# Kernel tuning notes

Hardware: AMD Instinct MI355X
Metric: run time of the kernel (lower is better)

## Reference

```python
import jax, jax.numpy as jnp
import numpy as np

EMBED_DIM = 1024
NUM_HEADS = 16
HEAD_DIM = EMBED_DIM // NUM_HEADS
SCALING = (1.0 / HEAD_DIM) ** 0.5


def setup_inputs() -> dict:
    key = jax.random.key(0)
    ks = jax.random.split(key, 9)
    d = EMBED_DIM
    return {
        "hidden_states": jax.random.normal(ks[0], (4, 2048, d), dtype=jnp.float32),
        "q_w": jax.random.normal(ks[1], (d, d), dtype=jnp.float32) * 0.02,
        "q_b": jax.random.normal(ks[2], (d,), dtype=jnp.float32) * 0.02,
        "k_w": jax.random.normal(ks[3], (d, d), dtype=jnp.float32) * 0.02,
        "k_b": jax.random.normal(ks[4], (d,), dtype=jnp.float32) * 0.02,
        "v_w": jax.random.normal(ks[5], (d, d), dtype=jnp.float32) * 0.02,
        "v_b": jax.random.normal(ks[6], (d,), dtype=jnp.float32) * 0.02,
        "out_w": jax.random.normal(ks[7], (d, d), dtype=jnp.float32) * 0.02,
        "out_b": jax.random.normal(ks[8], (d,), dtype=jnp.float32) * 0.02,
    }


def _shape(x, bsz, seq, nh, hd):
    # [B, T, E] -> [B, H, T, Hd]
    return x.reshape(bsz, seq, nh, hd).transpose(0, 2, 1, 3)


def reference(hidden_states, q_w, q_b, k_w, k_b, v_w, v_b, out_w, out_b):
    bsz, tgt_len, _ = hidden_states.shape
    # torch Linear: y = x @ W.T + b; query scaled by sqrt(1/head_dim)
    q = (hidden_states @ q_w.T + q_b) * SCALING
    k = hidden_states @ k_w.T + k_b
    v = hidden_states @ v_w.T + v_b
    q = _shape(q, bsz, tgt_len, NUM_HEADS, HEAD_DIM)
    k = _shape(k, bsz, tgt_len, NUM_HEADS, HEAD_DIM)
    v = _shape(v, bsz, tgt_len, NUM_HEADS, HEAD_DIM)
    # [B, H, T, S]
    attn_weights = jnp.einsum("bhtd,bhsd->bhts", q, k)
    attn_weights = jax.nn.softmax(attn_weights, axis=-1)
    # [B, H, T, Hd] -> [B, T, E]
    attn_output = jnp.einsum("bhts,bhsd->bhtd", attn_weights, v)
    attn_output = attn_output.transpose(0, 2, 1, 3).reshape(bsz, tgt_len, EMBED_DIM)
    return attn_output @ out_w.T + out_b
```

## Files before the change

kernel.cpp:

```cpp
#include <hip/hip_runtime.h>
#include <hip/hip_bf16.h>
#include <cstdint>
#include <math.h>

typedef uint16_t u16;
typedef __attribute__((ext_vector_type(8))) short short8;
typedef __attribute__((ext_vector_type(4))) float floatx4;
typedef __attribute__((ext_vector_type(16))) float floatx16;

__device__ __forceinline__ float bf2f(u16 u) {
  return __uint_as_float(((uint32_t)u) << 16);
}
__device__ __forceinline__ u16 f2bf(float f) {
  uint32_t u = __float_as_uint(f);
  u += 0x7FFF + ((u >> 16) & 1);
  return (u16)(u >> 16);
}

__device__ __forceinline__ void glds16(const void* g, void* l) {
  __builtin_amdgcn_global_load_lds(
      (const __attribute__((address_space(1))) void*)g,
      (__attribute__((address_space(3))) void*)l, 16, 0, 0);
}

__device__ __forceinline__ bool detect_fp32(const u16* __restrict__ hs) {
  int big = 0;
#pragma unroll
  for (int i = 0; i < 128; ++i) {
    const int e = (hs[i] >> 7) & 0xFF;
    big += (e >= 140);
  }
  return big > 0;
}

__device__ __forceinline__ void conv_blk(
    const void* __restrict__ src, u16* __restrict__ dst, int i, bool f32)
{
  if (f32) {
    const float4 v = ((const float4*)src)[i];
    ushort4 d;
    d.x = f2bf(v.x); d.y = f2bf(v.y); d.z = f2bf(v.z); d.w = f2bf(v.w);
    ((ushort4*)dst)[i] = d;
  } else {
    ((ushort4*)dst)[i] = ((const ushort4*)src)[i];
  }
}

__global__ __launch_bounds__(256) void convert_all(
    const void* __restrict__ hs, const void* __restrict__ qw,
    const void* __restrict__ kw, const void* __restrict__ vw,
    const void* __restrict__ ow, const void* __restrict__ qb,
    const void* __restrict__ kb, const void* __restrict__ vb,
    const void* __restrict__ ob,
    u16* __restrict__ d_hs, u16* __restrict__ d_qw, u16* __restrict__ d_kw,
    u16* __restrict__ d_vw, u16* __restrict__ d_ow, u16* __restrict__ d_qb,
    u16* __restrict__ d_kb, u16* __restrict__ d_vb, u16* __restrict__ d_ob)
{
  const bool f32 = detect_fp32((const u16*)hs);
  const int bid = blockIdx.x;
  const int tid = threadIdx.x;
  if (bid < 8192) {
    conv_blk(hs, d_hs, bid * 256 + tid, f32);
  } else if (bid < 8192 + 4096) {
    const int w = (bid - 8192) >> 10;
    const int i = ((bid - 8192) & 1023) * 256 + tid;
    const void* s = (w == 0) ? qw : (w == 1) ? kw : (w == 2) ? vw : ow;
    u16* d        = (w == 0) ? d_qw : (w == 1) ? d_kw : (w == 2) ? d_vw : d_ow;
    conv_blk(s, d, i, f32);
  } else {
    const int w = bid - 12288;
    const void* s = (w == 0) ? qb : (w == 1) ? kb : (w == 2) ? vb : ob;
    u16* d        = (w == 0) ? d_qb : (w == 1) ? d_kb : (w == 2) ? d_vb : d_ob;
    conv_blk(s, d, tid, f32);
  }
}

template <int MODE>
__device__ __forceinline__ void gemm_body(
    const u16* __restrict__ A, const u16* __restrict__ W,
    const u16* __restrict__ bias, void* __restrict__ vout,
    float scale, u16* As, u16* Bs, int bx, int by, bool f32out)
{
  constexpr int KD = 1024;
  const int tid  = threadIdx.x;
  const int lane = tid & 63;
  const int l15  = lane & 15;
  const int quad = lane >> 4;
  const int wid  = tid >> 6;
  const int bm = by * 128, bn = bx * 128;
  const int wm = (wid >> 1) * 64, wn = (wid & 1) * 64;

  floatx4 acc[4][4];
#pragma unroll
  for (int i = 0; i < 4; ++i)
#pragma unroll
    for (int j = 0; j < 4; ++j)
#pragma unroll
      for (int r = 0; r < 4; ++r) acc[i][j][r] = 0.0f;

  const int c0 = tid, c1 = tid + 256;
  const u16* Ag0 = A + (size_t)(bm + (c0 >> 2)) * KD + (c0 & 3) * 8;
  const u16* Ag1 = A + (size_t)(bm + (c1 >> 2)) * KD + (c1 & 3) * 8;
  const u16* Wg0 = W + (size_t)(bn + (c0 >> 2)) * KD + (c0 & 3) * 8;
  const u16* Wg1 = W + (size_t)(bn + (c1 >> 2)) * KD + (c1 & 3) * 8;
  u16* As0 = As + c0 * 8;  u16* As1 = As + c1 * 8;
  u16* Bs0 = Bs + c0 * 8;  u16* Bs1 = Bs + c1 * 8;

  for (int kt = 0; kt < KD / 32; ++kt) {
    const int ko = kt * 32;
    glds16(Ag0 + ko, As0);
    glds16(Ag1 + ko, As1);
    glds16(Wg0 + ko, Bs0);
    glds16(Wg1 + ko, Bs1);
    __syncthreads();
    short8 af[4], bf[4];
#pragma unroll
    for (int mb = 0; mb < 4; ++mb)
      af[mb] = *(const short8*)&As[(wm + mb * 16 + l15) * 32 + quad * 8];
#pragma unroll
    for (int nb = 0; nb < 4; ++nb)
      bf[nb] = *(const short8*)&Bs[(wn + nb * 16 + l15) * 32 + quad * 8];
#pragma unroll
    for (int mb = 0; mb < 4; ++mb)
#pragma unroll
      for (int nb = 0; nb < 4; ++nb) {
        if (MODE == 2)
          acc[mb][nb] = __builtin_amdgcn_mfma_f32_16x16x32_bf16(
              bf[nb], af[mb], acc[mb][nb], 0, 0, 0);
        else
          acc[mb][nb] = __builtin_amdgcn_mfma_f32_16x16x32_bf16(
              af[mb], bf[nb], acc[mb][nb], 0, 0, 0);
      }
    __syncthreads();
  }

  if (MODE == 2) {
#pragma unroll
    for (int nb = 0; nb < 4; ++nb)
#pragma unroll
      for (int r = 0; r < 4; ++r) {
        const int wrow = bn + wn + nb * 16 + quad * 4 + r;
        const float bv = bf2f(bias[wrow]);
        const int h = wrow >> 6, d = wrow & 63;
        u16* out = (u16*)vout;
#pragma unroll
        for (int mb = 0; mb < 4; ++mb) {
          const int tcol = bm + wm + mb * 16 + l15;
          const int b = tcol >> 11, t = tcol & 2047;
          out[((size_t)(b * 16 + h) * 64 + d) * 2048 + t] =
              f2bf((acc[mb][nb][r] + bv) * scale);
        }
      }
  } else {
    float bias_v[4];
#pragma unroll
    for (int nb = 0; nb < 4; ++nb) bias_v[nb] = bf2f(bias[bn + wn + nb * 16 + l15]);
#pragma unroll
    for (int mb = 0; mb < 4; ++mb)
#pragma unroll
      for (int nb = 0; nb < 4; ++nb)
#pragma unroll
        for (int r = 0; r < 4; ++r) {
          const int row = bm + wm + mb * 16 + quad * 4 + r;
          const int col = bn + wn + nb * 16 + l15;
          const float v = (acc[mb][nb][r] + bias_v[nb]) * scale;
          if (MODE == 0) {
            if (f32out) ((float*)vout)[(size_t)row * 1024 + col] = v;
            else        ((u16*)vout)[(size_t)row * 1024 + col] = f2bf(v);
          } else {
            const int b = row >> 11, t = row & 2047;
            const int h = col >> 6, d = col & 63;
            ((u16*)vout)[(((size_t)(b * 16 + h)) * 2048 + t) * 64 + d] = f2bf(v);
          }
        }
  }
}

__global__ __launch_bounds__(256, 3) void gemm_qkv(
    const u16* __restrict__ A,
    const u16* __restrict__ Wq, const u16* __restrict__ Wk, const u16* __restrict__ Wv,
    const u16* __restrict__ bq, const u16* __restrict__ bk, const u16* __restrict__ bv,
    u16* __restrict__ Oq, u16* __restrict__ Ok, u16* __restrict__ Ov)
{
  __shared__ u16 As[128 * 32];
  __shared__ u16 Bs[128 * 32];
  const int z = blockIdx.z;
  if (z < 2) {
    const u16* W    = z ? Wk : Wq;
    const u16* bias = z ? bk : bq;
    u16* out        = z ? Ok : Oq;
    const float scale = z ? 1.0f : 0.125f;
    gemm_body<1>(A, W, bias, out, scale, As, Bs, blockIdx.x, blockIdx.y, false);
  } else {
    gemm_body<2>(A, Wv, bv, Ov, 1.0f, As, Bs, blockIdx.x, blockIdx.y, false);
  }
}

__global__ __launch_bounds__(256, 3) void gemm_out_proj(
    const u16* __restrict__ A, const u16* __restrict__ W,
    const u16* __restrict__ bias, void* __restrict__ out,
    const u16* __restrict__ probe)
{
  __shared__ u16 As[128 * 32];
  __shared__ u16 Bs[128 * 32];
  const bool f32 = detect_fp32(probe);
  gemm_body<0>(A, W, bias, out, 1.0f, As, Bs, blockIdx.x, blockIdx.y, f32);
}

__global__ __launch_bounds__(256, 4) void attn_fused(
    const u16* __restrict__ Q, const u16* __restrict__ K,
    const u16* __restrict__ VT, u16* __restrict__ O)
{
  constexpr int T = 2048, D = 64;
  constexpr int KS = 72;
  constexpr int VS = 136;
  __shared__ u16 Ks[128 * KS];
  __shared__ u16 Vts[64 * VS];
  __shared__ float Linv[128];

  const int tid  = threadIdx.x;
  const int lane = tid & 63;
  const int l31  = lane & 31;
  const int half = lane >> 5;
  const int wid  = tid >> 6;
  const int bh = blockIdx.y;
  const int qt = blockIdx.x;
  const int q0w = wid * 32;

  const u16* Qb = Q + (size_t)bh * T * D + (size_t)qt * 128 * D;
  const u16* Kb = K + (size_t)bh * T * D;
  const u16* Vb = VT + (size_t)bh * D * T;

  short8 qf[4];
#pragma unroll
  for (int kk = 0; kk < 4; ++kk)
    qf[kk] = *(const short8*)&Qb[(q0w + l31) * D + kk * 16 + half * 8];

  floatx16 o_acc[2];
#pragma unroll
  for (int dt = 0; dt < 2; ++dt)
#pragma unroll
    for (int i = 0; i < 16; ++i) o_acc[dt][i] = 0.0f;
  float lA = 0.0f, lB = 0.0f;

#pragma unroll 1
  for (int kt = 0; kt < T / 128; ++kt) {
    const u16* Kt = Kb + (size_t)kt * 128 * D;
#pragma unroll
    for (int j = 0; j < 4; ++j) {
      const int c = tid + j * 256;
      const int r = c >> 3, d0 = (c & 7) * 8;
      *(short8*)&Ks[r * KS + d0] = *(const short8*)&Kt[r * D + d0];
    }
#pragma unroll
    for (int j = 0; j < 4; ++j) {
      const int c = tid + j * 256;
      const int d = c >> 4, toff = (c & 15) * 8;
      *(short8*)&Vts[d * VS + toff] =
          *(const short8*)&Vb[(size_t)d * T + kt * 128 + toff];
    }
    __syncthreads();

#pragma unroll
    for (int t = 0; t < 4; ++t) {
      floatx16 s;
#pragma unroll
      for (int i = 0; i < 16; ++i) s[i] = 0.0f;
#pragma unroll
      for (int kk = 0; kk < 4; ++kk) {
        const short8 kf = *(const short8*)&Ks[(t * 32 + l31) * KS + kk * 16 + half * 8];
        s = __builtin_amdgcn_mfma_f32_32x32x16_bf16(kf, qf[kk], s, 0, 0, 0);
      }
      uint32_t e[4][2];
#pragma unroll
      for (int g = 0; g < 4; ++g) {
        const float p0 = __expf(fminf((float)s[4 * g + 0], 30.f));
        const float p1 = __expf(fminf((float)s[4 * g + 1], 30.f));
        const float p2 = __expf(fminf((float)s[4 * g + 2], 30.f));
        const float p3 = __expf(fminf((float)s[4 * g + 3], 30.f));
        lA += p0 + p1;
        lB += p2 + p3;
        const uint32_t u0 = __float_as_uint(p0) + 0x8000u;
        const uint32_t u1 = __float_as_uint(p1) + 0x8000u;
        const uint32_t u2 = __float_as_uint(p2) + 0x8000u;
        const uint32_t u3 = __float_as_uint(p3) + 0x8000u;
        e[g][0] = __builtin_amdgcn_perm(u1, u0, 0x07060302);
        e[g][1] = __builtin_amdgcn_perm(u3, u2, 0x07060302);
      }
#pragma unroll
      for (int c = 0; c < 2; ++c) {
        const uint32_t x0 = half ? e[2 * c][0] : e[2 * c + 1][0];
        const uint32_t x1 = half ? e[2 * c][1] : e[2 * c + 1][1];
        const uint32_t r0 = (uint32_t)__shfl_xor((int)x0, 32);
        const uint32_t r1 = (uint32_t)__shfl_xor((int)x1, 32);
        union { uint32_t u[4]; short8 v; } pu;
        pu.u[0] = half ? r0 : e[2 * c][0];
        pu.u[1] = half ? r1 : e[2 * c][1];
        pu.u[2] = half ? e[2 * c + 1][0] : r0;
        pu.u[3] = half ? e[2 * c + 1][1] : r1;
        const short8 pf = pu.v;
        const int kkp = 2 * t + c;
        const short8 vf0 = *(const short8*)&Vts[l31 * VS + kkp * 16 + half * 8];
        const short8 vf1 = *(const short8*)&Vts[(32 + l31) * VS + kkp * 16 + half * 8];
        o_acc[0] = __builtin_amdgcn_mfma_f32_32x32x16_bf16(pf, vf0, o_acc[0], 0, 0, 0);
        o_acc[1] = __builtin_amdgcn_mfma_f32_32x32x16_bf16(pf, vf1, o_acc[1], 0, 0, 0);
      }
    }
    __syncthreads();
  }

  const float l_acc = lA + lB;
  const float l_full = l_acc + __shfl_xor(l_acc, 32);
  Linv[q0w + l31] = 1.0f / l_full;

  const int b = bh >> 4, h = bh & 15;
  u16* Ob = O + ((size_t)b * 2048 + (size_t)qt * 128) * 1024 + h * 64;
  float invs[16];
#pragma unroll
  for (int i = 0; i < 16; ++i)
    invs[i] = Linv[q0w + (i & 3) + 8 * (i >> 2) + 4 * half];
#pragma unroll
  for (int dt = 0; dt < 2; ++dt)
#pragma unroll
    for (int i = 0; i < 16; ++i) {
      const int qrow = q0w + (i & 3) + 8 * (i >> 2) + 4 * half;
      Ob[(size_t)qrow * 1024 + dt * 32 + l31] = f2bf((float)o_acc[dt][i] * invs[i]);
    }
}

extern "C" void kernel_launch(void* const* d_in, const int* in_sizes, int n_in,
                              void* d_out, int out_size, void* d_ws, size_t ws_size,
                              hipStream_t stream) {
  const u16* hs_probe = (const u16*)d_in[0];

  const size_t TE = (size_t)4 * 2048 * 1024;
  const size_t WE = (size_t)1024 * 1024;
  u16* hsB = (u16*)d_ws;
  u16* Qb  = hsB + TE;
  u16* Kb  = Qb + TE;
  u16* Vb  = Kb + TE;
  u16* Ob  = Vb + TE;
  u16* qwB = Ob + TE;
  u16* kwB = qwB + WE;
  u16* vwB = kwB + WE;
  u16* owB = vwB + WE;
  u16* qbB = owB + WE;
  u16* kbB = qbB + 1024;
  u16* vbB = kbB + 1024;
  u16* obB = vbB + 1024;

  dim3 bb(256);
  convert_all<<<dim3(12292), bb, 0, stream>>>(
      d_in[0], d_in[1], d_in[3], d_in[5], d_in[7],
      d_in[2], d_in[4], d_in[6], d_in[8],
      hsB, qwB, kwB, vwB, owB, qbB, kbB, vbB, obB);

  gemm_qkv<<<dim3(8, 64, 3), bb, 0, stream>>>(
      hsB, qwB, kwB, vwB, qbB, kbB, vbB, Qb, Kb, Vb);
  attn_fused<<<dim3(16, 64), bb, 0, stream>>>(Qb, Kb, Vb, Ob);
  gemm_out_proj<<<dim3(8, 64), bb, 0, stream>>>(Ob, owB, obB, d_out, hs_probe);
}
```

Before: 347.4 us.

## Double K-step in GEMMs, prefetch K/V to registers, fold log2e into Q scale

The projection GEMMs now load two 32-wide K slices per barrier pair into doubled LDS buffers, halving the number of syncs. The attention kernel prefetches the next K/V tile into registers while computing on the current one, overlapping global loads with MFMA work. The softmax exponent switches to a raw exp2 with the log2(e) factor folded into the query scale, dropping the clamp. This raises LDS use per block, which may lower occupancy, and removing the clamp risks overflow on large scores.

```diff
diff --git a/kernel.cpp b/kernel.cpp
--- a/kernel.cpp
+++ b/kernel.cpp
@@ -106,31 +106,36 @@
   u16* As0 = As + c0 * 8;  u16* As1 = As + c1 * 8;
   u16* Bs0 = Bs + c0 * 8;  u16* Bs1 = Bs + c1 * 8;
 
-  for (int kt = 0; kt < KD / 32; ++kt) {
-    const int ko = kt * 32;
-    glds16(Ag0 + ko, As0);
-    glds16(Ag1 + ko, As1);
-    glds16(Wg0 + ko, Bs0);
-    glds16(Wg1 + ko, Bs1);
+  for (int kt2 = 0; kt2 < KD / 64; ++kt2) {
+    const int ko0 = kt2 * 64, ko1 = ko0 + 32;
+    glds16(Ag0 + ko0, As0);        glds16(Ag1 + ko0, As1);
+    glds16(Wg0 + ko0, Bs0);        glds16(Wg1 + ko0, Bs1);
+    glds16(Ag0 + ko1, As0 + 4096); glds16(Ag1 + ko1, As1 + 4096);
+    glds16(Wg0 + ko1, Bs0 + 4096); glds16(Wg1 + ko1, Bs1 + 4096);
     __syncthreads();
-    short8 af[4], bf[4];
-#pragma unroll
-    for (int mb = 0; mb < 4; ++mb)
-      af[mb] = *(const short8*)&As[(wm + mb * 16 + l15) * 32 + quad * 8];
-#pragma unroll
-    for (int nb = 0; nb < 4; ++nb)
-      bf[nb] = *(const short8*)&Bs[(wn + nb * 16 + l15) * 32 + quad * 8];
-#pragma unroll
-    for (int mb = 0; mb < 4; ++mb)
-#pragma unroll
-      for (int nb = 0; nb < 4; ++nb) {
-        if (MODE == 2)
-          acc[mb][nb] = __builtin_amdgcn_mfma_f32_16x16x32_bf16(
-              bf[nb], af[mb], acc[mb][nb], 0, 0, 0);
-        else
-          acc[mb][nb] = __builtin_amdgcn_mfma_f32_16x16x32_bf16(
-              af[mb], bf[nb], acc[mb][nb], 0, 0, 0);
-      }
+#pragma unroll
+    for (int h = 0; h < 2; ++h) {
+      const u16* Ah = As + h * 4096;
+      const u16* Bh = Bs + h * 4096;
+      short8 af[4], bf[4];
+#pragma unroll
+      for (int mb = 0; mb < 4; ++mb)
+        af[mb] = *(const short8*)&Ah[(wm + mb * 16 + l15) * 32 + quad * 8];
+#pragma unroll
+      for (int nb = 0; nb < 4; ++nb)
+        bf[nb] = *(const short8*)&Bh[(wn + nb * 16 + l15) * 32 + quad * 8];
+#pragma unroll
+      for (int mb = 0; mb < 4; ++mb)
+#pragma unroll
+        for (int nb = 0; nb < 4; ++nb) {
+          if (MODE == 2)
+            acc[mb][nb] = __builtin_amdgcn_mfma_f32_16x16x32_bf16(
+                bf[nb], af[mb], acc[mb][nb], 0, 0, 0);
+          else
+            acc[mb][nb] = __builtin_amdgcn_mfma_f32_16x16x32_bf16(
+                af[mb], bf[nb], acc[mb][nb], 0, 0, 0);
+        }
+    }
     __syncthreads();
   }
 
@@ -182,14 +187,14 @@
     const u16* __restrict__ bq, const u16* __restrict__ bk, const u16* __restrict__ bv,
     u16* __restrict__ Oq, u16* __restrict__ Ok, u16* __restrict__ Ov)
 {
-  __shared__ u16 As[128 * 32];
-  __shared__ u16 Bs[128 * 32];
+  __shared__ u16 As[2 * 128 * 32];
+  __shared__ u16 Bs[2 * 128 * 32];
   const int z = blockIdx.z;
   if (z < 2) {
     const u16* W    = z ? Wk : Wq;
     const u16* bias = z ? bk : bq;
     u16* out        = z ? Ok : Oq;
-    const float scale = z ? 1.0f : 0.125f;
+    const float scale = z ? 1.0f : 0.18033688011112042f;
     gemm_body<1>(A, W, bias, out, scale, As, Bs, blockIdx.x, blockIdx.y, false);
   } else {
     gemm_body<2>(A, Wv, bv, Ov, 1.0f, As, Bs, blockIdx.x, blockIdx.y, false);
@@ -201,8 +206,8 @@
     const u16* __restrict__ bias, void* __restrict__ out,
     const u16* __restrict__ probe)
 {
-  __shared__ u16 As[128 * 32];
-  __shared__ u16 Bs[128 * 32];
+  __shared__ u16 As[2 * 128 * 32];
+  __shared__ u16 Bs[2 * 128 * 32];
   const bool f32 = detect_fp32(probe);
   gemm_body<0>(A, W, bias, out, 1.0f, As, Bs, blockIdx.x, blockIdx.y, f32);
 }
@@ -243,23 +248,33 @@
     for (int i = 0; i < 16; ++i) o_acc[dt][i] = 0.0f;
   float lA = 0.0f, lB = 0.0f;
 
+  short8 kreg[4], vreg[4];
+#pragma unroll
+  for (int j = 0; j < 4; ++j) {
+    const int c = tid + j * 256;
+    kreg[j] = *(const short8*)&Kb[(size_t)(c >> 3) * D + (c & 7) * 8];
+    vreg[j] = *(const short8*)&Vb[(size_t)(c >> 4) * T + (c & 15) * 8];
+  }
+
 #pragma unroll 1
   for (int kt = 0; kt < T / 128; ++kt) {
-    const u16* Kt = Kb + (size_t)kt * 128 * D;
 #pragma unroll
     for (int j = 0; j < 4; ++j) {
       const int c = tid + j * 256;
-      const int r = c >> 3, d0 = (c & 7) * 8;
-      *(short8*)&Ks[r * KS + d0] = *(const short8*)&Kt[r * D + d0];
-    }
-#pragma unroll
-    for (int j = 0; j < 4; ++j) {
-      const int c = tid + j * 256;
-      const int d = c >> 4, toff = (c & 15) * 8;
-      *(short8*)&Vts[d * VS + toff] =
-          *(const short8*)&Vb[(size_t)d * T + kt * 128 + toff];
+      *(short8*)&Ks[(c >> 3) * KS + (c & 7) * 8] = kreg[j];
+      *(short8*)&Vts[(c >> 4) * VS + (c & 15) * 8] = vreg[j];
     }
     __syncthreads();
+    if (kt + 1 < T / 128) {
+      const u16* Kn = Kb + (size_t)(kt + 1) * 128 * D;
+      const u16* Vn = Vb + (kt + 1) * 128;
+#pragma unroll
+      for (int j = 0; j < 4; ++j) {
+        const int c = tid + j * 256;
+        kreg[j] = *(const short8*)&Kn[(size_t)(c >> 3) * D + (c & 7) * 8];
+        vreg[j] = *(const short8*)&Vn[(size_t)(c >> 4) * T + (c & 15) * 8];
+      }
+    }
 
 #pragma unroll
     for (int t = 0; t < 4; ++t) {
@@ -274,10 +289,10 @@
       uint32_t e[4][2];
 #pragma unroll
       for (int g = 0; g < 4; ++g) {
-        const float p0 = __expf(fminf((float)s[4 * g + 0], 30.f));
-        const float p1 = __expf(fminf((float)s[4 * g + 1], 30.f));
-        const float p2 = __expf(fminf((float)s[4 * g + 2], 30.f));
-        const float p3 = __expf(fminf((float)s[4 * g + 3], 30.f));
+        const float p0 = __builtin_amdgcn_exp2f((float)s[4 * g + 0]);
+        const float p1 = __builtin_amdgcn_exp2f((float)s[4 * g + 1]);
+        const float p2 = __builtin_amdgcn_exp2f((float)s[4 * g + 2]);
+        const float p3 = __builtin_amdgcn_exp2f((float)s[4 * g + 3]);
         lA += p0 + p1;
         lB += p2 + p3;
         const uint32_t u0 = __float_as_uint(p0) + 0x8000u;
```

Measured after the change: 523.3 us. 50.6% more time.
